# Performance work log

Hardware: AMD Instinct MI355X
Metric: run time of the kernel (lower is better)

The kernel has to match this reference:

```python
import jax, jax.numpy as jnp
import numpy as np

V = 50000   # num_candidates
D = 32      # dim_item
B = 4096    # batch
N = 16      # max_n_node
L = 20      # max_session_length
STEPS = 1   # propagation_steps


def setup_inputs() -> dict:
    key = jax.random.key(0)
    ks = jax.random.split(key, 19)
    s = 1.0 / np.sqrt(D)
    u = lambda k, shp: jax.random.uniform(k, shp, jnp.float32, -s, s)
    return {
        "alias_inputs": jax.random.randint(ks[0], (B, L), 0, N),
        "A": jax.random.uniform(ks[1], (B, N, 2 * N), jnp.float32),
        "items": jax.random.randint(ks[2], (B, N), 0, V),
        "mask": jnp.ones((B, L), jnp.int32),
        "emb": u(ks[3], (V, D)),
        "w_ih": u(ks[4], (3 * D, 2 * D)),
        "w_hh": u(ks[5], (3 * D, D)),
        "b_ih": u(ks[6], (3 * D,)),
        "b_hh": u(ks[7], (3 * D,)),
        "b_iah": u(ks[8], (D,)),
        "b_oah": u(ks[9], (D,)),
        "w_ein": u(ks[10], (D, D)),
        "b_ein": u(ks[11], (D,)),
        "w_eout": u(ks[12], (D, D)),
        "b_eout": u(ks[13], (D,)),
        "w1": u(ks[14], (D, D)),
        "b1": u(ks[15], (D,)),
        "w2": u(ks[16], (D, D)),
        "b2": u(ks[17], (D,)),
        "w3": u(ks[18], (D, 1)),
    }


def reference(alias_inputs, A, items, mask, emb, w_ih, w_hh, b_ih, b_hh,
              b_iah, b_oah, w_ein, b_ein, w_eout, b_eout, w1, b1, w2, b2, w3):
    # item embedding lookup: [B, N, D]
    h = emb[items]
    n = A.shape[1]
    for _ in range(STEPS):
        node_in = h @ w_ein + b_ein
        node_out = h @ w_eout + b_eout
        # adjacency message passing (incoming / outgoing halves of A)
        input_in = jnp.matmul(A[:, :, :n], node_in) + b_iah
        input_out = jnp.matmul(A[:, :, n:2 * n], node_out) + b_oah
        inputs = jnp.concatenate([input_in, input_out], axis=-1)  # [B,N,2D]
        gi = inputs @ w_ih.T + b_ih   # [B,N,3D]
        gh = h @ w_hh.T + b_hh        # [B,N,3D]
        i_r, i_i, i_n = jnp.split(gi, 3, axis=-1)
        h_r, h_i, h_n = jnp.split(gh, 3, axis=-1)
        resetgate = jax.nn.sigmoid(i_r + h_r)
        inputgate = jax.nn.sigmoid(i_i + h_i)
        newgate = jnp.tanh(i_n + resetgate * h_n)
        h = newgate + inputgate * (h - newgate)
    # per-sample gather: seq_hidden[b, t] = h[b, alias_inputs[b, t]]
    seq = jnp.take_along_axis(h, alias_inputs[:, :, None], axis=1)  # [B,L,D]
    last = jnp.sum(mask, axis=1) - 1
    ht = seq[jnp.arange(seq.shape[0]), last]  # [B,D]
    q1 = (ht @ w1 + b1)[:, None, :]           # [B,1,D]
    q2 = seq @ w2 + b2                        # [B,L,D]
    alpha = jax.nn.sigmoid(q1 + q2) @ w3      # [B,L,1]
    s_g = jnp.sum(alpha * seq * mask[:, :, None].astype(seq.dtype), axis=1)
    scores = s_g @ emb[1:].T                  # [B, V-1]
    return scores
```

## Files before the change

kernel.cpp:

```cpp
#include <hip/hip_runtime.h>
#include <hip/hip_bf16.h>


#define B_BATCH 4096
#define N_NODE  16
#define L_SEQ   20
#define D_DIM   32
#define NV_OUT  49999
#define EMB_ROWS 50176

typedef float  f32x4  __attribute__((ext_vector_type(4)));
typedef float  f32x4u __attribute__((ext_vector_type(4), aligned(4)));
typedef __bf16 bf16x8 __attribute__((ext_vector_type(8)));

__device__ __forceinline__ float sigf(float x) {
    return 1.0f / (1.0f + __expf(-x));
}

__global__ __launch_bounds__(256) void session3_kernel(
    const int*   __restrict__ alias_inputs,
    const float* __restrict__ A,
    const int*   __restrict__ items,
    const int*   __restrict__ mask,
    const float* __restrict__ emb,
    const float* __restrict__ w_ih,
    const float* __restrict__ w_hh,
    const float* __restrict__ b_ih, const float* __restrict__ b_hh,
    const float* __restrict__ b_iah, const float* __restrict__ b_oah,
    const float* __restrict__ w_ein, const float* __restrict__ b_ein,
    const float* __restrict__ w_eout, const float* __restrict__ b_eout,
    const float* __restrict__ w1, const float* __restrict__ b1,
    const float* __restrict__ w2, const float* __restrict__ b2,
    const float* __restrict__ w3,
    __hip_bfloat16* __restrict__ sg_hi,
    __hip_bfloat16* __restrict__ sg_lo)
{
    const int b   = blockIdx.x;
    const int tid = threadIdx.x;
    const int g   = tid >> 5;
    const int d   = tid & 31;
    const int n0  = g, n1 = g + 8;

    __shared__ float h_s [N_NODE][D_DIM];
    __shared__ float A_s [N_NODE][2 * N_NODE];
    __shared__ float ni_s[N_NODE][D_DIM];
    __shared__ float no_s[N_NODE][D_DIM];
    __shared__ float ii_s[N_NODE][D_DIM];
    __shared__ float io_s[N_NODE][D_DIM];
    __shared__ float wih_s[96][66];
    __shared__ float whh_s[96][34];
    __shared__ float q1_s[D_DIM];
    __shared__ float alpha_s[L_SEQ];
    __shared__ int   last_s;

    for (int idx = tid; idx < 512; idx += 256) {
        const int n = idx >> 5, dd = idx & 31;
        const int it = items[b * N_NODE + n];
        h_s[n][dd] = emb[(size_t)it * D_DIM + dd];
        A_s[n][dd] = A[(size_t)b * 512 + idx];
    }
    for (int f = tid; f < 96 * 64; f += 256) wih_s[f >> 6][f & 63] = w_ih[f];
    for (int f = tid; f < 96 * 32; f += 256) whh_s[f >> 5][f & 31] = w_hh[f];
    __syncthreads();

    float ai0 = b_ein[d], ao0 = b_eout[d];
    float ai1 = ai0,      ao1 = ao0;
    #pragma unroll
    for (int kb = 0; kb < 8; ++kb) {
        const int k0 = kb * 4;
        const f32x4 h0v = *reinterpret_cast<const f32x4*>(&h_s[n0][k0]);
        const f32x4 h1v = *reinterpret_cast<const f32x4*>(&h_s[n1][k0]);
        #pragma unroll
        for (int j = 0; j < 4; ++j) {
            const int k = k0 + j;
            const float we = w_ein[k * 32 + d], wo = w_eout[k * 32 + d];
            ai0 += h0v[j] * we; ai1 += h1v[j] * we;
            ao0 += h0v[j] * wo; ao1 += h1v[j] * wo;
        }
    }
    ni_s[n0][d] = ai0; ni_s[n1][d] = ai1;
    no_s[n0][d] = ao0; no_s[n1][d] = ao1;
    __syncthreads();

    float iv0 = b_iah[d], ov0 = b_oah[d];
    float iv1 = iv0,      ov1 = ov0;
    #pragma unroll
    for (int mb = 0; mb < 4; ++mb) {
        const int m0 = mb * 4;
        const f32x4 a0i = *reinterpret_cast<const f32x4*>(&A_s[n0][m0]);
        const f32x4 a1i = *reinterpret_cast<const f32x4*>(&A_s[n1][m0]);
        const f32x4 a0o = *reinterpret_cast<const f32x4*>(&A_s[n0][N_NODE + m0]);
        const f32x4 a1o = *reinterpret_cast<const f32x4*>(&A_s[n1][N_NODE + m0]);
        #pragma unroll
        for (int j = 0; j < 4; ++j) {
            const int m = m0 + j;
            const float nim = ni_s[m][d], nom = no_s[m][d];
            iv0 += a0i[j] * nim;
            iv1 += a1i[j] * nim;
            ov0 += a0o[j] * nom;
            ov1 += a1o[j] * nom;
        }
    }
    ii_s[n0][d] = iv0; ii_s[n1][d] = iv1;
    io_s[n0][d] = ov0; io_s[n1][d] = ov1;
    __syncthreads();

    float r0 = b_ih[d] + b_hh[d],           r1 = r0;
    float i0 = b_ih[32 + d] + b_hh[32 + d], i1 = i0;
    float gn0 = b_ih[64 + d],               gn1 = gn0;
    float hn0 = b_hh[64 + d],               hn1 = hn0;
    #pragma unroll
    for (int kb = 0; kb < 8; ++kb) {
        const int k0 = kb * 4;
        const f32x4 a0v = *reinterpret_cast<const f32x4*>(&ii_s[n0][k0]);
        const f32x4 a1v = *reinterpret_cast<const f32x4*>(&ii_s[n1][k0]);
        const f32x4 o0v = *reinterpret_cast<const f32x4*>(&io_s[n0][k0]);
        const f32x4 o1v = *reinterpret_cast<const f32x4*>(&io_s[n1][k0]);
        const f32x4 h0v = *reinterpret_cast<const f32x4*>(&h_s[n0][k0]);
        const f32x4 h1v = *reinterpret_cast<const f32x4*>(&h_s[n1][k0]);
        #pragma unroll
        for (int j = 0; j < 4; ++j) {
            const int k = k0 + j;
            const float wri = wih_s[d][k],      wro = wih_s[d][32 + k];
            const float wii = wih_s[32 + d][k], wio = wih_s[32 + d][32 + k];
            const float wni = wih_s[64 + d][k], wno = wih_s[64 + d][32 + k];
            const float whr = whh_s[d][k];
            const float whi = whh_s[32 + d][k];
            const float whn = whh_s[64 + d][k];
            r0  += a0v[j] * wri + o0v[j] * wro + h0v[j] * whr;
            r1  += a1v[j] * wri + o1v[j] * wro + h1v[j] * whr;
            i0  += a0v[j] * wii + o0v[j] * wio + h0v[j] * whi;
            i1  += a1v[j] * wii + o1v[j] * wio + h1v[j] * whi;
            gn0 += a0v[j] * wni + o0v[j] * wno;
            gn1 += a1v[j] * wni + o1v[j] * wno;
            hn0 += h0v[j] * whn;
            hn1 += h1v[j] * whn;
        }
    }

    float hv0, hv1;
    {
        const float rg0 = sigf(r0), ig0 = sigf(i0);
        const float x0  = gn0 + rg0 * hn0;
        const float e0  = __expf(2.0f * fabsf(x0));
        const float ng0 = copysignf(1.0f - 2.0f / (e0 + 1.0f), x0);
        hv0 = ng0 + ig0 * (h_s[n0][d] - ng0);
        const float rg1 = sigf(r1), ig1 = sigf(i1);
        const float x1  = gn1 + rg1 * hn1;
        const float e1  = __expf(2.0f * fabsf(x1));
        const float ng1 = copysignf(1.0f - 2.0f / (e1 + 1.0f), x1);
        hv1 = ng1 + ig1 * (h_s[n1][d] - ng1);
    }
    __syncthreads();
    h_s[n0][d] = hv0;
    h_s[n1][d] = hv1;
    __syncthreads();

    for (int idx = tid; idx < L_SEQ * D_DIM; idx += 256) {
        const int t = idx >> 5, dd = idx & 31;
        const int a = alias_inputs[b * L_SEQ + t];
        const float v = h_s[a][dd];
        if (t < 16) ni_s[t][dd] = v;
        else        no_s[t - 16][dd] = v;
    }
    if (tid == 0) {
        int s = 0;
        for (int t = 0; t < L_SEQ; ++t) s += mask[b * L_SEQ + t];
        last_s = s - 1;
    }
    __syncthreads();

    if (tid < D_DIM) {
        const int lt = last_s;
        const float* sl = (lt < 16) ? &ni_s[lt][0] : &no_s[lt - 16][0];
        float acc = b1[tid];
        #pragma unroll
        for (int k = 0; k < 32; ++k) acc += sl[k] * w1[k * 32 + tid];
        q1_s[tid] = acc;
    }
    __syncthreads();

    for (int idx = tid; idx < L_SEQ * D_DIM; idx += 256) {
        const int t = idx >> 5, dd = idx & 31;
        const float* sp = (t < 16) ? &ni_s[t][0] : &no_s[t - 16][0];
        float q2 = b2[dd];
        #pragma unroll
        for (int k = 0; k < 32; ++k) q2 += sp[k] * w2[k * 32 + dd];
        const float val = sigf(q1_s[dd] + q2) * w3[dd];
        if (t < 16) ii_s[t][dd] = val;
        else        io_s[t - 16][dd] = val;
    }
    __syncthreads();
    if (tid < L_SEQ) {
        const float* tp = (tid < 16) ? &ii_s[tid][0] : &io_s[tid - 16][0];
        float a = 0.0f;
        #pragma unroll
        for (int dd = 0; dd < 32; ++dd) a += tp[dd];
        alpha_s[tid] = a * (float)mask[b * L_SEQ + tid];
    }
    __syncthreads();

    if (tid < D_DIM) {
        float acc = 0.0f;
        #pragma unroll
        for (int t = 0; t < L_SEQ; ++t) {
            const float sv = (t < 16) ? ni_s[t][tid] : no_s[t - 16][tid];
            acc += alpha_s[t] * sv;
        }
        const __hip_bfloat16 h = __float2bfloat16(acc);
        sg_hi[b * D_DIM + tid] = h;
        sg_lo[b * D_DIM + tid] = __float2bfloat16(acc - __bfloat162float(h));
    }
}

__global__ __launch_bounds__(256) void conv_emb_kernel(
    const float* __restrict__ emb, __hip_bfloat16* __restrict__ emb_b)
{
    const int total = EMB_ROWS * D_DIM;
    for (int i = blockIdx.x * 256 + threadIdx.x; i < total; i += gridDim.x * 256) {
        const int v = i >> 5, k = i & 31;
        int src = v + 1;
        if (src > NV_OUT) src = NV_OUT;
        emb_b[i] = __float2bfloat16(emb[(size_t)src * D_DIM + k]);
    }
}

__global__ __launch_bounds__(256) void score8_kernel(
    const __hip_bfloat16* __restrict__ sg_hi,
    const __hip_bfloat16* __restrict__ sg_lo,
    const __hip_bfloat16* __restrict__ emb_b,
    float* __restrict__ out)
{
    __shared__ float T[16][260];
    const int wave = threadIdx.x >> 6;
    const int lane = threadIdx.x & 63;
    const int rc   = lane & 15;
    const int kgrp = lane >> 4;
    const int b0   = blockIdx.y * 16;
    const int v0   = blockIdx.x * 256;
    const int vw   = v0 + wave * 64;

    const bf16x8 ah = *reinterpret_cast<const bf16x8*>(
        &sg_hi[(size_t)(b0 + rc) * D_DIM + kgrp * 8]);
    const bf16x8 al = *reinterpret_cast<const bf16x8*>(
        &sg_lo[(size_t)(b0 + rc) * D_DIM + kgrp * 8]);

    #pragma unroll
    for (int s = 0; s < 4; ++s) {
        const int vt = vw + s * 16;
        const bf16x8 bf = *reinterpret_cast<const bf16x8*>(
            &emb_b[(size_t)(vt + rc) * D_DIM + kgrp * 8]);
        f32x4 acc = {0.0f, 0.0f, 0.0f, 0.0f};
        acc = __builtin_amdgcn_mfma_f32_16x16x32_bf16(ah, bf, acc, 0, 0, 0);
        acc = __builtin_amdgcn_mfma_f32_16x16x32_bf16(al, bf, acc, 0, 0, 0);
        const int col = wave * 64 + s * 16 + rc;
        #pragma unroll
        for (int j = 0; j < 4; ++j)
            T[kgrp * 4 + j][col] = acc[j];
    }
    __syncthreads();

    if (v0 + 256 <= NV_OUT) {
        #pragma unroll
        for (int r = 0; r < 4; ++r) {
            const int row = wave * 4 + r;
            const f32x4 val = *reinterpret_cast<const f32x4*>(&T[row][lane * 4]);
            f32x4u* op = reinterpret_cast<f32x4u*>(
                &out[(size_t)(b0 + row) * NV_OUT + v0 + lane * 4]);
            __builtin_nontemporal_store(val, op);
        }
    } else {
        #pragma unroll
        for (int r = 0; r < 4; ++r) {
            const int row = wave * 4 + r;
            float* op = &out[(size_t)(b0 + row) * NV_OUT];
            #pragma unroll
            for (int j = 0; j < 4; ++j) {
                const int c = lane * 4 + j;
                if (v0 + c < NV_OUT) op[v0 + c] = T[row][c];
            }
        }
    }
}

extern "C" void kernel_launch(void* const* d_in, const int* in_sizes, int n_in,
                              void* d_out, int out_size, void* d_ws, size_t ws_size,
                              hipStream_t stream)
{
    const int*   alias_inputs = (const int*)  d_in[0];
    const float* A      = (const float*)d_in[1];
    const int*   items  = (const int*)  d_in[2];
    const int*   mask   = (const int*)  d_in[3];
    const float* emb    = (const float*)d_in[4];
    const float* w_ih   = (const float*)d_in[5];
    const float* w_hh   = (const float*)d_in[6];
    const float* b_ih   = (const float*)d_in[7];
    const float* b_hh   = (const float*)d_in[8];
    const float* b_iah  = (const float*)d_in[9];
    const float* b_oah  = (const float*)d_in[10];
    const float* w_ein  = (const float*)d_in[11];
    const float* b_ein  = (const float*)d_in[12];
    const float* w_eout = (const float*)d_in[13];
    const float* b_eout = (const float*)d_in[14];
    const float* w1     = (const float*)d_in[15];
    const float* b1     = (const float*)d_in[16];
    const float* w2     = (const float*)d_in[17];
    const float* b2     = (const float*)d_in[18];
    const float* w3     = (const float*)d_in[19];

    __hip_bfloat16* sg_hi = (__hip_bfloat16*)((char*)d_ws + 512 * 1024);
    __hip_bfloat16* sg_lo = (__hip_bfloat16*)((char*)d_ws + 768 * 1024);
    __hip_bfloat16* emb_b = (__hip_bfloat16*)((char*)d_ws + 1024 * 1024);
    float* out = (float*)d_out;

    hipLaunchKernelGGL(conv_emb_kernel, dim3(2048), dim3(256), 0, stream,
                       emb, emb_b);

    hipLaunchKernelGGL(session3_kernel, dim3(B_BATCH), dim3(256), 0, stream,
                       alias_inputs, A, items, mask, emb,
                       w_ih, w_hh, b_ih, b_hh, b_iah, b_oah,
                       w_ein, b_ein, w_eout, b_eout,
                       w1, b1, w2, b2, w3, sg_hi, sg_lo);

    hipLaunchKernelGGL(score8_kernel,
                       dim3((NV_OUT + 255) / 256, B_BATCH / 16),
                       dim3(256), 0, stream, sg_hi, sg_lo, emb_b, out);
}
```

Before: 313.2 us.

## Fold embedding conversion into session kernel and double score-tile width per block

```diff
diff --git a/kernel.cpp b/kernel.cpp
--- a/kernel.cpp
+++ b/kernel.cpp
@@ -8,6 +8,7 @@
 #define D_DIM   32
 #define NV_OUT  49999
 #define EMB_ROWS 50176
+#define CONV_BLOCKS 392
 
 typedef float  f32x4  __attribute__((ext_vector_type(4)));
 typedef float  f32x4u __attribute__((ext_vector_type(4), aligned(4)));
@@ -17,7 +18,7 @@
     return 1.0f / (1.0f + __expf(-x));
 }
 
-__global__ __launch_bounds__(256) void session3_kernel(
+__global__ __launch_bounds__(256) void session_conv_kernel(
     const int*   __restrict__ alias_inputs,
     const float* __restrict__ A,
     const int*   __restrict__ items,
@@ -33,10 +34,25 @@
     const float* __restrict__ w2, const float* __restrict__ b2,
     const float* __restrict__ w3,
     __hip_bfloat16* __restrict__ sg_hi,
-    __hip_bfloat16* __restrict__ sg_lo)
+    __hip_bfloat16* __restrict__ sg_lo,
+    __hip_bfloat16* __restrict__ emb_b)
 {
+    const int tid = threadIdx.x;
+
+    if (blockIdx.x >= B_BATCH) {
+        const int base = (blockIdx.x - B_BATCH) * 4096 + tid;
+        #pragma unroll
+        for (int it = 0; it < 16; ++it) {
+            const int i = base + it * 256;
+            const int v = i >> 5, k = i & 31;
+            int src = v + 1;
+            if (src > NV_OUT) src = NV_OUT;
+            emb_b[i] = __float2bfloat16(emb[(size_t)src * D_DIM + k]);
+        }
+        return;
+    }
+
     const int b   = blockIdx.x;
-    const int tid = threadIdx.x;
     const int g   = tid >> 5;
     const int d   = tid & 31;
     const int n0  = g, n1 = g + 8;
@@ -213,19 +229,7 @@
     }
 }
 
-__global__ __launch_bounds__(256) void conv_emb_kernel(
-    const float* __restrict__ emb, __hip_bfloat16* __restrict__ emb_b)
-{
-    const int total = EMB_ROWS * D_DIM;
-    for (int i = blockIdx.x * 256 + threadIdx.x; i < total; i += gridDim.x * 256) {
-        const int v = i >> 5, k = i & 31;
-        int src = v + 1;
-        if (src > NV_OUT) src = NV_OUT;
-        emb_b[i] = __float2bfloat16(emb[(size_t)src * D_DIM + k]);
-    }
-}
-
-__global__ __launch_bounds__(256) void score8_kernel(
+__global__ __launch_bounds__(256) void score10_kernel(
     const __hip_bfloat16* __restrict__ sg_hi,
     const __hip_bfloat16* __restrict__ sg_lo,
     const __hip_bfloat16* __restrict__ emb_b,
@@ -237,8 +241,7 @@
     const int rc   = lane & 15;
     const int kgrp = lane >> 4;
     const int b0   = blockIdx.y * 16;
-    const int v0   = blockIdx.x * 256;
-    const int vw   = v0 + wave * 64;
+    const int vbase = blockIdx.x * 512;
 
     const bf16x8 ah = *reinterpret_cast<const bf16x8*>(
         &sg_hi[(size_t)(b0 + rc) * D_DIM + kgrp * 8]);
@@ -246,40 +249,47 @@
         &sg_lo[(size_t)(b0 + rc) * D_DIM + kgrp * 8]);
 
     #pragma unroll
-    for (int s = 0; s < 4; ++s) {
-        const int vt = vw + s * 16;
-        const bf16x8 bf = *reinterpret_cast<const bf16x8*>(
-            &emb_b[(size_t)(vt + rc) * D_DIM + kgrp * 8]);
-        f32x4 acc = {0.0f, 0.0f, 0.0f, 0.0f};
-        acc = __builtin_amdgcn_mfma_f32_16x16x32_bf16(ah, bf, acc, 0, 0, 0);
-        acc = __builtin_amdgcn_mfma_f32_16x16x32_bf16(al, bf, acc, 0, 0, 0);
-        const int col = wave * 64 + s * 16 + rc;
-        #pragma unroll
-        for (int j = 0; j < 4; ++j)
-            T[kgrp * 4 + j][col] = acc[j];
-    }
-    __syncthreads();
-
-    if (v0 + 256 <= NV_OUT) {
-        #pragma unroll
-        for (int r = 0; r < 4; ++r) {
-            const int row = wave * 4 + r;
-            const f32x4 val = *reinterpret_cast<const f32x4*>(&T[row][lane * 4]);
-            f32x4u* op = reinterpret_cast<f32x4u*>(
-                &out[(size_t)(b0 + row) * NV_OUT + v0 + lane * 4]);
-            __builtin_nontemporal_store(val, op);
-        }
-    } else {
-        #pragma unroll
-        for (int r = 0; r < 4; ++r) {
-            const int row = wave * 4 + r;
-            float* op = &out[(size_t)(b0 + row) * NV_OUT];
+    for (int half = 0; half < 2; ++half) {
+        const int v0 = vbase + half * 256;
+        const int vw = v0 + wave * 64;
+
+        #pragma unroll
+        for (int s = 0; s < 4; ++s) {
+            const int vt = vw + s * 16;
+            const bf16x8 bf = *reinterpret_cast<const bf16x8*>(
+                &emb_b[(size_t)(vt + rc) * D_DIM + kgrp * 8]);
+            f32x4 acc = {0.0f, 0.0f, 0.0f, 0.0f};
+            acc = __builtin_amdgcn_mfma_f32_16x16x32_bf16(ah, bf, acc, 0, 0, 0);
+            acc = __builtin_amdgcn_mfma_f32_16x16x32_bf16(al, bf, acc, 0, 0, 0);
+            const int col = wave * 64 + s * 16 + rc;
             #pragma unroll
-            for (int j = 0; j < 4; ++j) {
-                const int c = lane * 4 + j;
-                if (v0 + c < NV_OUT) op[v0 + c] = T[row][c];
+            for (int j = 0; j < 4; ++j)
+                T[kgrp * 4 + j][col] = acc[j];
+        }
+        __syncthreads();
+
+        if (v0 + 256 <= NV_OUT) {
+            #pragma unroll
+            for (int r = 0; r < 4; ++r) {
+                const int row = wave * 4 + r;
+                const f32x4 val = *reinterpret_cast<const f32x4*>(&T[row][lane * 4]);
+                f32x4u* op = reinterpret_cast<f32x4u*>(
+                    &out[(size_t)(b0 + row) * NV_OUT + v0 + lane * 4]);
+                __builtin_nontemporal_store(val, op);
             }
-        }
+        } else {
+            #pragma unroll
+            for (int r = 0; r < 4; ++r) {
+                const int row = wave * 4 + r;
+                float* op = &out[(size_t)(b0 + row) * NV_OUT];
+                #pragma unroll
+                for (int j = 0; j < 4; ++j) {
+                    const int c = lane * 4 + j;
+                    if (v0 + c < NV_OUT) op[v0 + c] = T[row][c];
+                }
+            }
+        }
+        __syncthreads();
     }
 }
 
@@ -313,16 +323,14 @@
     __hip_bfloat16* emb_b = (__hip_bfloat16*)((char*)d_ws + 1024 * 1024);
     float* out = (float*)d_out;
 
-    hipLaunchKernelGGL(conv_emb_kernel, dim3(2048), dim3(256), 0, stream,
-                       emb, emb_b);
-
-    hipLaunchKernelGGL(session3_kernel, dim3(B_BATCH), dim3(256), 0, stream,
+    hipLaunchKernelGGL(session_conv_kernel, dim3(B_BATCH + CONV_BLOCKS),
+                       dim3(256), 0, stream,
                        alias_inputs, A, items, mask, emb,
                        w_ih, w_hh, b_ih, b_hh, b_iah, b_oah,
                        w_ein, b_ein, w_eout, b_eout,
-                       w1, b1, w2, b2, w3, sg_hi, sg_lo);
-
-    hipLaunchKernelGGL(score8_kernel,
-                       dim3((NV_OUT + 255) / 256, B_BATCH / 16),
+                       w1, b1, w2, b2, w3, sg_hi, sg_lo, emb_b);
+
+    hipLaunchKernelGGL(score10_kernel,
+                       dim3((NV_OUT + 511) / 512, B_BATCH / 16),
                        dim3(256), 0, stream, sg_hi, sg_lo, emb_b, out);
 }
```

New measurement: 316.1 us. Within noise of the previous version (+0.9%).
